# Kernel optimization log

Hardware: AMD Instinct MI355X
Metric: run time of the kernel (lower is better)

## Reference

```python
import jax, jax.numpy as jnp
import numpy as np

EMBED_DIM = 768
NUM_HEADS = 12
HEAD_DIM = EMBED_DIM // NUM_HEADS


def setup_inputs() -> dict:
    key = jax.random.key(0)
    k_x, k_wqkv, k_bqkv, k_wo, k_bo = jax.random.split(key, 5)
    B, S, D = 4, 2048, EMBED_DIM
    bound = 1.0 / np.sqrt(D)
    x = jax.random.normal(k_x, (B, S, D), dtype=jnp.float32)
    # nn.Linear weights: torch stores [out, in]; we keep same layout and use x @ W.T
    W_qkv = jax.random.uniform(k_wqkv, (3 * D, D), jnp.float32, -bound, bound)
    b_qkv = jax.random.uniform(k_bqkv, (3 * D,), jnp.float32, -bound, bound)
    W_out = jax.random.uniform(k_wo, (D, D), jnp.float32, -bound, bound)
    b_out = jax.random.uniform(k_bo, (D,), jnp.float32, -bound, bound)
    return {"x": x, "W_qkv": W_qkv, "b_qkv": b_qkv, "W_out": W_out, "b_out": b_out}


def reference(x, W_qkv, b_qkv, W_out, b_out):
    B, S, D = x.shape
    H, Hd = NUM_HEADS, HEAD_DIM
    qkv = x @ W_qkv.T + b_qkv                       # [B,S,3D]
    qkv = qkv.reshape(B, S, H, 3 * Hd).transpose(0, 2, 1, 3)  # [B,H,S,3Hd]
    q, k, v = jnp.split(qkv, 3, axis=-1)            # each [B,H,S,Hd]
    scale = Hd ** -0.5
    scores = jnp.einsum("bhsd,bhtd->bhst", q, k) * scale  # [B,H,S,S]
    weights = jax.nn.softmax(scores, axis=-1)
    ctx = jnp.einsum("bhst,bhtd->bhsd", weights, v)       # [B,H,S,Hd]
    ctx = ctx.transpose(0, 2, 1, 3).reshape(B, S, D)      # [B,S,D]
    return ctx @ W_out.T + b_out
```

## Files before the change

kernel.cpp:

```cpp
#include <hip/hip_runtime.h>
#include <hip/hip_bf16.h>
#include <stdint.h>
#include <math.h>

typedef unsigned short u16;
typedef __attribute__((ext_vector_type(8))) short short8;
typedef __attribute__((ext_vector_type(4))) float f32x4;
typedef __attribute__((ext_vector_type(16))) float f32x16;
typedef __attribute__((ext_vector_type(4))) unsigned int u32x4;
typedef __attribute__((ext_vector_type(2))) unsigned int u32x2;

#define NB 4
#define NS 2048
#define NH 12
#define HD 64
#define ND 768
#define ND3 2304

#define QSCALE 0.18033688f

__device__ __forceinline__ u16 f2bf(float f) {
    unsigned int u = __float_as_uint(f);
    unsigned int r = u + 0x7fffu + ((u >> 16) & 1u);
    return (u16)(r >> 16);
}

__device__ __forceinline__ void gload16(const u16* g, u16* s) {
    __builtin_amdgcn_global_load_lds(
        (const __attribute__((address_space(1))) unsigned int*)(const void*)g,
        (__attribute__((address_space(3))) unsigned int*)(void*)s, 16, 0, 0);
}

__device__ __forceinline__ unsigned int cvtpk(float lo, float hi) {
    unsigned int pk;
    asm("v_cvt_pk_bf16_f32 %0, %1, %2" : "=v"(pk) : "v"(lo), "v"(hi));
    return pk;
}

#define XN4   1572864
#define WQN4  442368
#define WON4  147456
__global__ __launch_bounds__(256) void castall(const float* __restrict__ x,
                                               const float* __restrict__ wq,
                                               const float* __restrict__ wo,
                                               u16* __restrict__ xb,
                                               u16* __restrict__ wqb,
                                               u16* __restrict__ wob) {
    int i = blockIdx.x * 256 + threadIdx.x;
    const float* s; u16* d; int j;
    if (i < XN4) { s = x; d = xb; j = i; }
    else if (i < XN4 + WQN4) { s = wq; d = wqb; j = i - XN4; }
    else if (i < XN4 + WQN4 + WON4) { s = wo; d = wob; j = i - XN4 - WQN4; }
    else return;
    float4 v = ((const float4*)s)[j];
    ushort4 o;
    o.x = f2bf(v.x); o.y = f2bf(v.y); o.z = f2bf(v.z); o.w = f2bf(v.w);
    ((ushort4*)d)[j] = o;
}

__global__ __launch_bounds__(256, 2) void gemm_qkv(const u16* __restrict__ A,
                                                   const u16* __restrict__ Bw,
                                                   const float* __restrict__ bias,
                                                   u16* __restrict__ Qg,
                                                   u16* __restrict__ Kg,
                                                   u16* __restrict__ Vtg) {
    __shared__ u16 lds[2][20480];
    const int tid = threadIdx.x;
    const int w = tid >> 6, l = tid & 63;
    const int lam = l & 15, quad = l >> 4;
    const int wm = w >> 1, wn = w & 1;
    const int bm = blockIdx.x * 128;
    const int hh = blockIdx.y;
    const int bn = hh * 192;
    const int NT = ND / 64;

    f32x4 acc[4][6];
#pragma unroll
    for (int i = 0; i < 4; i++)
#pragma unroll
        for (int j = 0; j < 6; j++) { f32x4 z = {0.f, 0.f, 0.f, 0.f}; acc[i][j] = z; }

    const u16* gp[10];
    int so[10];
#pragma unroll
    for (int i = 0; i < 10; i++) {
        int c = w * 10 + i;
        so[i] = c * 512;
        if (c < 16) {
            int rowgrp = c >> 1, ks = c & 1;
            gp[i] = A + (size_t)(bm + rowgrp * 16 + lam) * ND + ks * 32 + quad * 8;
        } else {
            int cc = c - 16, nf = cc >> 1, ks = cc & 1;
            gp[i] = Bw + (size_t)(bn + nf * 16 + lam) * ND + ks * 32 + quad * 8;
        }
    }

#pragma unroll
    for (int i = 0; i < 10; i++) gload16(gp[i], &lds[0][so[i]]);

    for (int t = 0; t < NT; ++t) {
        asm volatile("s_waitcnt vmcnt(0)" ::: "memory");
        __builtin_amdgcn_s_barrier();
        asm volatile("" ::: "memory");
        if (t + 1 < NT) {
#pragma unroll
            for (int i = 0; i < 10; i++) gload16(gp[i] + (t + 1) * 64, &lds[(t + 1) & 1][so[i]]);
        }
        const u16* buf = lds[t & 1];
#pragma unroll
        for (int ks = 0; ks < 2; ks++) {
            short8 a[4];
#pragma unroll
            for (int i = 0; i < 4; i++) a[i] = *(const short8*)(buf + ((wm * 4 + i) * 2 + ks) * 512 + l * 8);
#pragma unroll
            for (int half = 0; half < 2; half++) {
                short8 b[3];
#pragma unroll
                for (int j = 0; j < 3; j++) b[j] = *(const short8*)(buf + (16 + (wn * 6 + half * 3 + j) * 2 + ks) * 512 + l * 8);
#pragma unroll
                for (int mf = 0; mf < 4; mf++)
#pragma unroll
                    for (int j = 0; j < 3; j++)
                        acc[mf][half * 3 + j] = __builtin_amdgcn_mfma_f32_16x16x32_bf16(a[mf], b[j], acc[mf][half * 3 + j], 0, 0, 0);
            }
        }
    }

    u16* ctqk = &lds[0][0];
    u16* ctv  = &lds[0][0] + 128 * 136;
    __syncthreads();

#pragma unroll
    for (int nf = 0; nf < 6; nf++) {
        int nloc = wn * 96 + nf * 16;
        int rgn = nloc / 64;
        float bv = bias[bn + nloc + lam];
        if (rgn == 2) {
            int d = (nloc - 128) + lam;
#pragma unroll
            for (int mf = 0; mf < 4; mf++) {
                int s_local = wm * 64 + mf * 16 + quad * 4;
                ushort4 o;
                o.x = f2bf(acc[mf][nf][0] + bv);
                o.y = f2bf(acc[mf][nf][1] + bv);
                o.z = f2bf(acc[mf][nf][2] + bv);
                o.w = f2bf(acc[mf][nf][3] + bv);
                *(ushort4*)(ctv + d * 140 + s_local) = o;
            }
        } else {
            int col = nloc + lam;
            const float sc = (rgn == 0) ? QSCALE : 1.0f;
#pragma unroll
            for (int mf = 0; mf < 4; mf++)
#pragma unroll
                for (int r = 0; r < 4; r++) {
                    int row = wm * 64 + mf * 16 + quad * 4 + r;
                    ctqk[row * 136 + col] = f2bf((acc[mf][nf][r] + bv) * sc);
                }
        }
    }
    __syncthreads();

    const int bq = bm >> 11, s0g = bm & 2047;
    const size_t qkbase = ((size_t)(bq * NH + hh) * NS + s0g) * HD;
    const size_t vbase  = ((size_t)(bq * NH + hh) * HD) * NS + s0g;
#pragma unroll
    for (int p = 0; p < 8; p++) {
        int li = p * 256 + tid;
        {
            int row = li >> 4, u = li & 15;
            ushort4 v = *(const ushort4*)(ctqk + row * 136 + u * 4);
            *(ushort4*)(Qg + qkbase + (size_t)row * HD + u * 4) = v;
        }
        {
            int row = li >> 4, u = li & 15;
            ushort4 v = *(const ushort4*)(ctqk + row * 136 + 64 + u * 4);
            *(ushort4*)(Kg + qkbase + (size_t)row * HD + u * 4) = v;
        }
        {
            int d = li >> 5, u = li & 31;
            ushort4 v = *(const ushort4*)(ctv + d * 140 + u * 4);
            *(ushort4*)(Vtg + vbase + (size_t)d * NS + u * 4) = v;
        }
    }
}

__global__ __launch_bounds__(256, 3) void attn(const u16* __restrict__ Qg,
                                               const u16* __restrict__ Kg,
                                               const u16* __restrict__ Vtg,
                                               u16* __restrict__ ctx) {
    __shared__ u16 kv_lds[3][8192];
    const int tid = threadIdx.x;
    const int w = tid >> 6, L = tid & 63;
    const int r5 = L & 31, h = L >> 5;
    const int bid = blockIdx.x;
    const int qt = bid / 48, bh = bid % 48;
    const int b = bh / NH, hd = bh % NH;
    const u16* Qh = Qg + (size_t)bh * NS * HD;
    const u16* Kh = Kg + (size_t)bh * NS * HD;
    const u16* Vh = Vtg + (size_t)bh * HD * NS;

    const int qbase = qt * 128 + w * 32;

    short8 qf[4];
#pragma unroll
    for (int s = 0; s < 4; s++)
        qf[s] = *(const short8*)(Qh + (size_t)(qbase + r5) * HD + s * 16 + h * 8);

    f32x16 ot[2];
#pragma unroll
    for (int hg = 0; hg < 2; hg++)
#pragma unroll
        for (int r = 0; r < 16; r++) ot[hg][r] = 0.f;

    f32x16 lsum;
#pragma unroll
    for (int r = 0; r < 16; r++) lsum[r] = 0.f;
    short8 onesf;
#pragma unroll
    for (int i = 0; i < 8; i++) onesf[i] = (short)0x3F80;

    f32x16 zero16;
#pragma unroll
    for (int r = 0; r < 16; r++) zero16[r] = 0.f;
    asm volatile("" : "+v"(zero16));

    const u16* gp[4];
    int so[4];
    int step;
    if (w < 2) {
#pragma unroll
        for (int i = 0; i < 4; i++) {
            int c = w * 4 + i;
            int kg = c >> 2, s = c & 3;
            gp[i] = Kh + (size_t)(kg * 32 + r5) * HD + s * 16 + h * 8;
            so[i] = c * 512;
        }
        step = 64 * HD;
    } else {
#pragma unroll
        for (int i = 0; i < 4; i++) {
            int v = (w - 2) * 4 + i;
            int hg = v >> 2, tb = v & 3;
            gp[i] = Vh + (size_t)(hg * 32 + r5) * NS + tb * 16 + h * 8;
            so[i] = (8 + v) * 512;
        }
        step = 64;
    }

    const int NT = NS / 64;
#pragma unroll
    for (int t = 0; t < 2; t++)
#pragma unroll
        for (int i = 0; i < 4; i++) gload16(gp[i] + (size_t)t * step, &kv_lds[t][so[i]]);

    int cur = 0, nx2 = 2;
    for (int kt = 0; kt < NT; kt++) {
        if (kt < NT - 1) asm volatile("s_waitcnt vmcnt(4)" ::: "memory");
        else             asm volatile("s_waitcnt vmcnt(0)" ::: "memory");
        __builtin_amdgcn_s_barrier();
        asm volatile("" ::: "memory");
        if (kt + 2 < NT) {
#pragma unroll
            for (int i = 0; i < 4; i++) gload16(gp[i] + (size_t)(kt + 2) * step, &kv_lds[nx2][so[i]]);
        }
        const u16* buf = kv_lds[cur];

#pragma unroll
        for (int kg = 0; kg < 2; kg++) {
            short8 kf0 = *(const short8*)(buf + (kg * 4 + 0) * 512 + L * 8);
            f32x16 st = __builtin_amdgcn_mfma_f32_32x32x16_bf16(kf0, qf[0], zero16, 0, 0, 0);
#pragma unroll
            for (int s = 1; s < 4; s++) {
                short8 kf = *(const short8*)(buf + (kg * 4 + s) * 512 + L * 8);
                st = __builtin_amdgcn_mfma_f32_32x32x16_bf16(kf, qf[s], st, 0, 0, 0);
            }

            float e[16];
#pragma unroll
            for (int i = 0; i < 16; i++) e[i] = __builtin_amdgcn_exp2f(st[i]);
            unsigned int q8[8];
#pragma unroll
            for (int i = 0; i < 8; i++) q8[i] = cvtpk(e[2 * i], e[2 * i + 1]);

            u32x2 s02 = __builtin_amdgcn_permlane32_swap(q8[0], q8[2], false, false);
            u32x2 s13 = __builtin_amdgcn_permlane32_swap(q8[1], q8[3], false, false);
            u32x2 s46 = __builtin_amdgcn_permlane32_swap(q8[4], q8[6], false, false);
            u32x2 s57 = __builtin_amdgcn_permlane32_swap(q8[5], q8[7], false, false);
            union { u32x4 u; short8 s; } af0, af1;
            af0.u = (u32x4){s02.x, s13.x, s02.y, s13.y};
            af1.u = (u32x4){s46.x, s57.x, s46.y, s57.y};

            lsum = __builtin_amdgcn_mfma_f32_32x32x16_bf16(af0.s, onesf, lsum, 0, 0, 0);
            lsum = __builtin_amdgcn_mfma_f32_32x32x16_bf16(af1.s, onesf, lsum, 0, 0, 0);
#pragma unroll
            for (int hg = 0; hg < 2; hg++) {
                short8 vf0 = *(const short8*)(buf + (8 + hg * 4 + kg * 2 + 0) * 512 + L * 8);
                short8 vf1 = *(const short8*)(buf + (8 + hg * 4 + kg * 2 + 1) * 512 + L * 8);
                ot[hg] = __builtin_amdgcn_mfma_f32_32x32x16_bf16(af0.s, vf0, ot[hg], 0, 0, 0);
                ot[hg] = __builtin_amdgcn_mfma_f32_32x32x16_bf16(af1.s, vf1, ot[hg], 0, 0, 0);
            }
        }
        cur = (cur == 2) ? 0 : cur + 1;
        nx2 = (nx2 == 2) ? 0 : nx2 + 1;
    }

    float inv[16];
#pragma unroll
    for (int r = 0; r < 16; r++) inv[r] = __builtin_amdgcn_rcpf(lsum[r]);
#pragma unroll
    for (int hg = 0; hg < 2; hg++) {
#pragma unroll
        for (int r = 0; r < 16; r++) {
            int q = qbase + (r & 3) + 8 * (r >> 2) + 4 * h;
            ctx[(size_t)(b * NS + q) * ND + hd * HD + hg * 32 + r5] = f2bf(ot[hg][r] * inv[r]);
        }
    }
}

__global__ __launch_bounds__(256, 2) void gemm_out(const u16* __restrict__ A,
                                                   const u16* __restrict__ Bw,
                                                   const float* __restrict__ bias,
                                                   float* __restrict__ out) {
    __shared__ u16 lds[2][14336];
    const int tid = threadIdx.x;
    const int w = tid >> 6, l = tid & 63;
    const int lam = l & 15, quad = l >> 4;
    const int wm = w >> 1, wn = w & 1;
    const int bm = blockIdx.x * 128, bn = blockIdx.y * 96;
    const int NT = ND / 64;

    f32x4 acc[4][3];
#pragma unroll
    for (int i = 0; i < 4; i++)
#pragma unroll
        for (int j = 0; j < 3; j++) { f32x4 z = {0.f, 0.f, 0.f, 0.f}; acc[i][j] = z; }

    const u16* gp[7];
    int so[7];
#pragma unroll
    for (int i = 0; i < 7; i++) {
        int c = w * 7 + i;
        so[i] = c * 512;
        if (c < 16) {
            int rowgrp = c >> 1, ks = c & 1;
            gp[i] = A + (size_t)(bm + rowgrp * 16 + lam) * ND + ks * 32 + quad * 8;
        } else {
            int cc = c - 16, nf = cc >> 1, ks = cc & 1;
            gp[i] = Bw + (size_t)(bn + nf * 16 + lam) * ND + ks * 32 + quad * 8;
        }
    }

#pragma unroll
    for (int i = 0; i < 7; i++) gload16(gp[i], &lds[0][so[i]]);

    for (int t = 0; t < NT; ++t) {
        asm volatile("s_waitcnt vmcnt(0)" ::: "memory");
        __builtin_amdgcn_s_barrier();
        asm volatile("" ::: "memory");
        if (t + 1 < NT) {
#pragma unroll
            for (int i = 0; i < 7; i++) gload16(gp[i] + (t + 1) * 64, &lds[(t + 1) & 1][so[i]]);
        }
        const u16* buf = lds[t & 1];
#pragma unroll
        for (int ks = 0; ks < 2; ks++) {
            short8 a[4], b[3];
#pragma unroll
            for (int i = 0; i < 4; i++) a[i] = *(const short8*)(buf + ((wm * 4 + i) * 2 + ks) * 512 + l * 8);
#pragma unroll
            for (int j = 0; j < 3; j++) b[j] = *(const short8*)(buf + (16 + (wn * 3 + j) * 2 + ks) * 512 + l * 8);
#pragma unroll
            for (int mf = 0; mf < 4; mf++)
#pragma unroll
                for (int j = 0; j < 3; j++)
                    acc[mf][j] = __builtin_amdgcn_mfma_f32_16x16x32_bf16(a[mf], b[j], acc[mf][j], 0, 0, 0);
        }
    }

#pragma unroll
    for (int nf = 0; nf < 3; nf++) {
        int n = bn + wn * 48 + nf * 16 + lam;
        float bv = bias[n];
#pragma unroll
        for (int mf = 0; mf < 4; mf++)
#pragma unroll
            for (int r = 0; r < 4; r++) {
                int m = bm + wm * 64 + mf * 16 + quad * 4 + r;
                out[(size_t)m * ND + n] = acc[mf][nf][r] + bv;
            }
    }
}

extern "C" void kernel_launch(void* const* d_in, const int* in_sizes, int n_in,
                              void* d_out, int out_size, void* d_ws, size_t ws_size,
                              hipStream_t stream) {
    const float* x    = (const float*)d_in[0];
    const float* Wqkv = (const float*)d_in[1];
    const float* bqkv = (const float*)d_in[2];
    const float* Wout = (const float*)d_in[3];
    const float* bout = (const float*)d_in[4];
    float* out = (float*)d_out;

    u16* p = (u16*)d_ws;
    u16* xb    = p; p += 6291456;
    u16* wqkvb = p; p += 1769472;
    u16* wob   = p; p += 589824;
    u16* Qg    = p; p += 6291456;
    u16* Kg    = p; p += 6291456;
    u16* Vtg   = p; p += 6291456;
    u16* ctx   = p; p += 6291456;

    castall<<<8448, 256, 0, stream>>>(x, Wqkv, Wout, xb, wqkvb, wob);
    gemm_qkv<<<dim3(64, 12), 256, 0, stream>>>(xb, wqkvb, bqkv, Qg, Kg, Vtg);
    attn<<<768, 256, 0, stream>>>(Qg, Kg, Vtg, ctx);
    gemm_out<<<dim3(64, 8), 256, 0, stream>>>(ctx, wob, bout, out);
}
```

Baseline: 218.4 us.

## Load K/V fragments directly from global memory in attention, drop LDS pipeline

Removes the triple-buffered LDS staging of K and V tiles, along with its async global-to-LDS loads, waitcnts and barriers. Each wave now reads its K and V MFMA fragments straight from global memory. Occupancy is raised to 4 blocks per SM. This drops LDS traffic and block-wide synchronisation, but the four waves in a block each re-read the same K/V data from global memory or cache, and global load latency is no longer hidden by explicit prefetching.

```diff
diff --git a/kernel.cpp b/kernel.cpp
--- a/kernel.cpp
+++ b/kernel.cpp
@@ -185,11 +185,10 @@
     }
 }
 
-__global__ __launch_bounds__(256, 3) void attn(const u16* __restrict__ Qg,
+__global__ __launch_bounds__(256, 4) void attn(const u16* __restrict__ Qg,
                                                const u16* __restrict__ Kg,
                                                const u16* __restrict__ Vtg,
                                                u16* __restrict__ ctx) {
-    __shared__ u16 kv_lds[3][8192];
     const int tid = threadIdx.x;
     const int w = tid >> 6, L = tid & 63;
     const int r5 = L & 31, h = L >> 5;
@@ -225,54 +224,18 @@
     for (int r = 0; r < 16; r++) zero16[r] = 0.f;
     asm volatile("" : "+v"(zero16));
 
-    const u16* gp[4];
-    int so[4];
-    int step;
-    if (w < 2) {
-#pragma unroll
-        for (int i = 0; i < 4; i++) {
-            int c = w * 4 + i;
-            int kg = c >> 2, s = c & 3;
-            gp[i] = Kh + (size_t)(kg * 32 + r5) * HD + s * 16 + h * 8;
-            so[i] = c * 512;
-        }
-        step = 64 * HD;
-    } else {
-#pragma unroll
-        for (int i = 0; i < 4; i++) {
-            int v = (w - 2) * 4 + i;
-            int hg = v >> 2, tb = v & 3;
-            gp[i] = Vh + (size_t)(hg * 32 + r5) * NS + tb * 16 + h * 8;
-            so[i] = (8 + v) * 512;
-        }
-        step = 64;
-    }
-
-    const int NT = NS / 64;
-#pragma unroll
-    for (int t = 0; t < 2; t++)
-#pragma unroll
-        for (int i = 0; i < 4; i++) gload16(gp[i] + (size_t)t * step, &kv_lds[t][so[i]]);
-
-    int cur = 0, nx2 = 2;
-    for (int kt = 0; kt < NT; kt++) {
-        if (kt < NT - 1) asm volatile("s_waitcnt vmcnt(4)" ::: "memory");
-        else             asm volatile("s_waitcnt vmcnt(0)" ::: "memory");
-        __builtin_amdgcn_s_barrier();
-        asm volatile("" ::: "memory");
-        if (kt + 2 < NT) {
-#pragma unroll
-            for (int i = 0; i < 4; i++) gload16(gp[i] + (size_t)(kt + 2) * step, &kv_lds[nx2][so[i]]);
-        }
-        const u16* buf = kv_lds[cur];
-
+    const u16* kbase = Kh + (size_t)r5 * HD + h * 8;
+    const u16* vbase = Vh + (size_t)r5 * NS + h * 8;
+
+    for (int kt = 0; kt < 32; kt++) {
 #pragma unroll
         for (int kg = 0; kg < 2; kg++) {
-            short8 kf0 = *(const short8*)(buf + (kg * 4 + 0) * 512 + L * 8);
+            const u16* kp = kbase + (size_t)(kt * 64 + kg * 32) * HD;
+            short8 kf0 = *(const short8*)(kp);
             f32x16 st = __builtin_amdgcn_mfma_f32_32x32x16_bf16(kf0, qf[0], zero16, 0, 0, 0);
 #pragma unroll
             for (int s = 1; s < 4; s++) {
-                short8 kf = *(const short8*)(buf + (kg * 4 + s) * 512 + L * 8);
+                short8 kf = *(const short8*)(kp + s * 16);
                 st = __builtin_amdgcn_mfma_f32_32x32x16_bf16(kf, qf[s], st, 0, 0, 0);
             }
 
@@ -295,14 +258,13 @@
             lsum = __builtin_amdgcn_mfma_f32_32x32x16_bf16(af1.s, onesf, lsum, 0, 0, 0);
 #pragma unroll
             for (int hg = 0; hg < 2; hg++) {
-                short8 vf0 = *(const short8*)(buf + (8 + hg * 4 + kg * 2 + 0) * 512 + L * 8);
-                short8 vf1 = *(const short8*)(buf + (8 + hg * 4 + kg * 2 + 1) * 512 + L * 8);
+                const u16* vp = vbase + (size_t)hg * 32 * NS + kt * 64 + kg * 32;
+                short8 vf0 = *(const short8*)(vp);
+                short8 vf1 = *(const short8*)(vp + 16);
                 ot[hg] = __builtin_amdgcn_mfma_f32_32x32x16_bf16(af0.s, vf0, ot[hg], 0, 0, 0);
                 ot[hg] = __builtin_amdgcn_mfma_f32_32x32x16_bf16(af1.s, vf1, ot[hg], 0, 0, 0);
             }
         }
-        cur = (cur == 2) ? 0 : cur + 1;
-        nx2 = (nx2 == 2) ? 0 : nx2 + 1;
     }
 
     float inv[16];
```

Measured after the change: 335.8 us. +53.8%, slower.
